# Kernel tuning notes

Hardware: AMD Instinct MI355X
Metric: run time of the kernel (lower is better)

The kernel has to match this reference:

```python
import jax, jax.numpy as jnp
import numpy as np

B, S, D, H = 2, 2048, 1024, 16
HD = D // H  # head dim = 64


def setup_inputs() -> dict:
    key = jax.random.key(0)
    ks = jax.random.split(key, 5)
    scale = 1.0 / np.sqrt(D)
    return {
        "hidden_states": jax.random.normal(ks[0], (B, S, D), jnp.float32),
        "attention_mask": jax.random.normal(ks[1], (B, 1, 1, S), jnp.float32),
        "Wq": jax.random.normal(ks[2], (D, D), jnp.float32) * scale,
        "bq": jnp.zeros((D,), jnp.float32),
        "Wk": jax.random.normal(ks[3], (D, D), jnp.float32) * scale,
        "bk": jnp.zeros((D,), jnp.float32),
        "Wv": jax.random.normal(ks[4], (D, D), jnp.float32) * scale,
        "bv": jnp.zeros((D,), jnp.float32),
    }


def _split_heads(x):
    # [B,S,D] -> [B,H,S,HD]
    return x.reshape(B, S, H, HD).transpose(0, 2, 1, 3)


def reference(hidden_states, attention_mask, Wq, bq, Wk, bk, Wv, bv):
    # torch Linear: y = x @ W.T + b
    q = _split_heads(hidden_states @ Wq.T + bq)
    k = _split_heads(hidden_states @ Wk.T + bk)
    v = _split_heads(hidden_states @ Wv.T + bv)

    scores = jnp.einsum("bhqd,bhkd->bhqk", q, k)
    # Faithful to source: with a mask present, the 1/sqrt(head_dim) scaling
    # is overwritten and raw scores are multiplied by the binary key mask.
    mask = (attention_mask >= 0).astype(scores.dtype)  # [B,1,1,S]
    probs = scores * mask
    # dropout prob = 0 (eval) -> identity

    ctx = jnp.einsum("bhqk,bhkd->bhqd", probs, v)
    ctx = ctx.transpose(0, 2, 1, 3).reshape(B, S, D)
    return ctx
```

## Files before the change

kernel.cpp:

```cpp
#include <hip/hip_runtime.h>

#define BB 2
#define SS 2048
#define DD 1024
#define HH 16
#define HDIM 64
#define MTOT 4096

typedef unsigned short u16;
typedef __bf16 bf16_t;
typedef bf16_t bf16x8 __attribute__((ext_vector_type(8)));
typedef float floatx4 __attribute__((ext_vector_type(4)));
typedef float floatx16 __attribute__((ext_vector_type(16)));

__device__ __forceinline__ float bf2f(u16 u) {
  union { unsigned int i; float f; } x;
  x.i = ((unsigned int)u) << 16;
  return x.f;
}
__device__ __forceinline__ u16 f2bf(float f) {
  union { float f; unsigned int i; } x;
  x.f = f;
  unsigned int r = x.i + 0x7fffu + ((x.i >> 16) & 1u);
  return (u16)(r >> 16);
}

__device__ __forceinline__ void gload16(const u16* g, u16* l) {
  __builtin_amdgcn_global_load_lds(
      (const __attribute__((address_space(1))) unsigned int*)g,
      (__attribute__((address_space(3))) unsigned int*)l, 16, 0, 0);
}

__global__ __launch_bounds__(256) void cast_to_bf16(
    const float* __restrict__ hs, const float* __restrict__ wq,
    const float* __restrict__ wk, const float* __restrict__ wv,
    u16* __restrict__ hs_b, u16* __restrict__ wq_b,
    u16* __restrict__ wk_b, u16* __restrict__ wv_b) {
  int fid = blockIdx.x * 256 + threadIdx.x;
  const float* src;
  u16* dst;
  int local;
  if (fid < 1048576) { src = hs; dst = hs_b; local = fid; }
  else if (fid < 1310720) { src = wq; dst = wq_b; local = fid - 1048576; }
  else if (fid < 1572864) { src = wk; dst = wk_b; local = fid - 1310720; }
  else { src = wv; dst = wv_b; local = fid - 1572864; }
  float4 v = reinterpret_cast<const float4*>(src)[local];
  ushort4 o;
  o.x = f2bf(v.x); o.y = f2bf(v.y); o.z = f2bf(v.z); o.w = f2bf(v.w);
  reinterpret_cast<ushort4*>(dst)[local] = o;
}

#define BKK 32
__global__ __launch_bounds__(256) void qkv_gemm_kernel(
    const u16* __restrict__ A,
    const u16* __restrict__ Wq, const u16* __restrict__ Wk, const u16* __restrict__ Wv,
    const float* __restrict__ bq, const float* __restrict__ bk, const float* __restrict__ bv,
    u16* __restrict__ Qo, u16* __restrict__ Ko, u16* __restrict__ Vo) {
  __shared__ u16 sA[128 * BKK];
  __shared__ u16 sB[128 * BKK];
  const int mt = blockIdx.y, ntall = blockIdx.x;
  const int seg = ntall >> 3, nt = ntall & 7;
  const u16* Wp = (seg == 0) ? Wq : (seg == 1) ? Wk : Wv;
  const float* bp = (seg == 0) ? bq : (seg == 1) ? bk : bv;
  u16* Out = (seg == 0) ? Qo : (seg == 1) ? Ko : Vo;
  const int m0 = mt * 128, n0 = nt * 128;
  const int tid = threadIdx.x;
  const int lane = tid & 63, wave = tid >> 6;
  const int wm = (wave >> 1) * 64, wn = (wave & 1) * 64;
  const int l32 = lane & 31, khalf = lane >> 5;
  const int grow = wave * 32 + l32;
  const int gcol = khalf * 8;
  floatx16 acc[2][2] = {};
  for (int k0 = 0; k0 < DD; k0 += BKK) {
#pragma unroll
    for (int c = 0; c < 2; ++c) {
      gload16(A + (size_t)(m0 + grow) * DD + k0 + c * 16 + gcol,
              sA + (wave * 128 + c * 64 + lane) * 8);
      gload16(Wp + (size_t)(n0 + grow) * DD + k0 + c * 16 + gcol,
              sB + (wave * 128 + c * 64 + lane) * 8);
    }
    __syncthreads();
#pragma unroll
    for (int kk = 0; kk < 2; ++kk) {
      bf16x8 af[2], bfr[2];
#pragma unroll
      for (int i = 0; i < 2; ++i) {
        int gA = (wave >> 1) * 2 + i;
        af[i] = *reinterpret_cast<const bf16x8*>(sA + (gA * 128 + kk * 64 + lane) * 8);
      }
#pragma unroll
      for (int j = 0; j < 2; ++j) {
        int gB = (wave & 1) * 2 + j;
        bfr[j] = *reinterpret_cast<const bf16x8*>(sB + (gB * 128 + kk * 64 + lane) * 8);
      }
#pragma unroll
      for (int i = 0; i < 2; ++i)
#pragma unroll
        for (int j = 0; j < 2; ++j)
          acc[i][j] = __builtin_amdgcn_mfma_f32_32x32x16_bf16(af[i], bfr[j], acc[i][j], 0, 0, 0);
    }
    __syncthreads();
  }
#pragma unroll
  for (int j = 0; j < 2; ++j) {
    int col = n0 + wn + j * 32 + l32;
    float bias = bp[col];
#pragma unroll
    for (int i = 0; i < 2; ++i) {
#pragma unroll
      for (int reg = 0; reg < 16; ++reg) {
        int row = m0 + wm + i * 32 + (reg & 3) + 8 * (reg >> 2) + 4 * khalf;
        Out[(size_t)row * DD + col] = f2bf(acc[i][j][reg] + bias);
      }
    }
  }
}

__global__ __launch_bounds__(256) void m_partial_kernel(
    const u16* __restrict__ Kb, const u16* __restrict__ Vb,
    const float* __restrict__ am, float* __restrict__ mpart) {
  __shared__ float sK[64 * 68];
  __shared__ float sV[64 * 68];
  const int bh = blockIdx.y;
  const int b = bh >> 4, h = bh & 15;
  const int tid = threadIdx.x;
  const int e0 = (tid & 15) * 4, d0 = (tid >> 4) * 4;
  float acc[4][4] = {};
  for (int cs = 0; cs < 4; ++cs) {
    const int s0 = (blockIdx.x * 4 + cs) * 64;
    if (cs) __syncthreads();
#pragma unroll
    for (int c = 0; c < 2; ++c) {
      int L = tid + c * 256;
      int srow = L >> 3;
      int col = (L & 7) * 8;
      size_t g = (size_t)(b * SS + s0 + srow) * DD + h * HDIM + col;
      uint4 kraw = *reinterpret_cast<const uint4*>(Kb + g);
      uint4 vraw = *reinterpret_cast<const uint4*>(Vb + g);
      float m = (am[b * SS + s0 + srow] >= 0.f) ? 1.f : 0.f;
      unsigned int kw[4] = {kraw.x, kraw.y, kraw.z, kraw.w};
      unsigned int vw[4] = {vraw.x, vraw.y, vraw.z, vraw.w};
#pragma unroll
      for (int q = 0; q < 4; ++q) {
        sK[srow * 68 + col + 2 * q]     = m * bf2f((u16)(kw[q] & 0xffffu));
        sK[srow * 68 + col + 2 * q + 1] = m * bf2f((u16)(kw[q] >> 16));
        sV[srow * 68 + col + 2 * q]     = bf2f((u16)(vw[q] & 0xffffu));
        sV[srow * 68 + col + 2 * q + 1] = bf2f((u16)(vw[q] >> 16));
      }
    }
    __syncthreads();
    for (int s = 0; s < 64; ++s) {
      float4 kk = *reinterpret_cast<const float4*>(&sK[s * 68 + e0]);
      float4 vv = *reinterpret_cast<const float4*>(&sV[s * 68 + d0]);
      float ka[4] = {kk.x, kk.y, kk.z, kk.w};
      float va[4] = {vv.x, vv.y, vv.z, vv.w};
#pragma unroll
      for (int i = 0; i < 4; ++i)
#pragma unroll
        for (int j = 0; j < 4; ++j) acc[i][j] += ka[i] * va[j];
    }
  }
  float* outp = mpart + ((size_t)(blockIdx.x * 32 + bh)) * 4096;
#pragma unroll
  for (int i = 0; i < 4; ++i) {
    float4 o = {acc[i][0], acc[i][1], acc[i][2], acc[i][3]};
    *reinterpret_cast<float4*>(&outp[(e0 + i) * 64 + d0]) = o;
  }
}

__global__ __launch_bounds__(256) void ctx_kernel(
    const u16* __restrict__ Qb, const float* __restrict__ mpart, float* __restrict__ Out) {
  __shared__ float sM[64 * 68];
  __shared__ float sQ[64 * 68];
  const int mchunk = blockIdx.x;
  const int h = blockIdx.y;
  const int m0 = mchunk * 64;
  const int b = m0 >> 11;
  const int bh = b * HH + h;
  const int tid = threadIdx.x;
#pragma unroll
  for (int c = 0; c < 4; ++c) {
    int L4 = c * 256 + tid;
    float4 s = {0.f, 0.f, 0.f, 0.f};
#pragma unroll
    for (int pc = 0; pc < 8; ++pc) {
      const float4* p4 = reinterpret_cast<const float4*>(mpart + ((size_t)(pc * 32 + bh)) * 4096);
      float4 t = p4[L4];
      s.x += t.x; s.y += t.y; s.z += t.z; s.w += t.w;
    }
    int e = L4 >> 4, d = (L4 & 15) * 4;
    *reinterpret_cast<float4*>(&sM[e * 68 + d]) = s;
  }
#pragma unroll
  for (int c = 0; c < 2; ++c) {
    int L = tid + c * 256;
    int row = L >> 3, col = (L & 7) * 8;
    uint4 q = *reinterpret_cast<const uint4*>(Qb + (size_t)(m0 + row) * DD + h * HDIM + col);
    unsigned int w[4] = {q.x, q.y, q.z, q.w};
#pragma unroll
    for (int t = 0; t < 4; ++t) {
      sQ[row * 68 + col + 2 * t]     = bf2f((u16)(w[t] & 0xffffu));
      sQ[row * 68 + col + 2 * t + 1] = bf2f((u16)(w[t] >> 16));
    }
  }
  __syncthreads();
  const int d0 = (tid & 15) * 4, ml0 = (tid >> 4) * 4;
  float acc[4][4] = {};
  for (int e4 = 0; e4 < 64; e4 += 4) {
    float4 mm[4], qq[4];
#pragma unroll
    for (int t = 0; t < 4; ++t)
      mm[t] = *reinterpret_cast<const float4*>(&sM[(e4 + t) * 68 + d0]);
#pragma unroll
    for (int i = 0; i < 4; ++i)
      qq[i] = *reinterpret_cast<const float4*>(&sQ[(ml0 + i) * 68 + e4]);
    float ma[4][4], qa[4][4];
#pragma unroll
    for (int t = 0; t < 4; ++t) {
      ma[t][0] = mm[t].x; ma[t][1] = mm[t].y; ma[t][2] = mm[t].z; ma[t][3] = mm[t].w;
      qa[t][0] = qq[t].x; qa[t][1] = qq[t].y; qa[t][2] = qq[t].z; qa[t][3] = qq[t].w;
    }
#pragma unroll
    for (int i = 0; i < 4; ++i)
#pragma unroll
      for (int t = 0; t < 4; ++t)
#pragma unroll
        for (int j = 0; j < 4; ++j)
          acc[i][j] += qa[i][t] * ma[t][j];
  }
#pragma unroll
  for (int i = 0; i < 4; ++i) {
    float4 o = {acc[i][0], acc[i][1], acc[i][2], acc[i][3]};
    *reinterpret_cast<float4*>(Out + (size_t)(m0 + ml0 + i) * DD + h * HDIM + d0) = o;
  }
}

extern "C" void kernel_launch(void* const* d_in, const int* in_sizes, int n_in,
                              void* d_out, int out_size, void* d_ws, size_t ws_size,
                              hipStream_t stream) {
  const float* hs = (const float*)d_in[0];
  const float* am = (const float*)d_in[1];
  const float* wq = (const float*)d_in[2];
  const float* bq = (const float*)d_in[3];
  const float* wk = (const float*)d_in[4];
  const float* bk = (const float*)d_in[5];
  const float* wv = (const float*)d_in[6];
  const float* bv = (const float*)d_in[7];
  float* out = (float*)d_out;
  char* ws = (char*)d_ws;

  u16* hs_b = (u16*)(ws);
  u16* wq_b = (u16*)(ws + 8388608);
  u16* wk_b = (u16*)(ws + 10485760);
  u16* wv_b = (u16*)(ws + 12582912);
  u16* q_b  = (u16*)(ws + 14680064);
  u16* k_b  = (u16*)(ws + 23068672);
  u16* v_b  = (u16*)(ws + 31457280);
  float* mpart = (float*)(ws + 39845888);

  cast_to_bf16<<<7168, 256, 0, stream>>>(hs, wq, wk, wv, hs_b, wq_b, wk_b, wv_b);
  qkv_gemm_kernel<<<dim3(24, 32), 256, 0, stream>>>(hs_b, wq_b, wk_b, wv_b,
                                                    bq, bk, bv, q_b, k_b, v_b);
  m_partial_kernel<<<dim3(8, 32), 256, 0, stream>>>(k_b, v_b, am, mpart);
  ctx_kernel<<<dim3(64, 16), 256, 0, stream>>>(q_b, mpart, out);
}
```

Measured before the change: 173.9 us.

## Cast inputs into k-panel layout for contiguous GEMM tile loads

The cast kernel now transposes the bf16 copies of hidden states and weights through shared memory into a panel layout ([K/8][rows][8]). The QKV GEMM loads each 16-byte k-chunk for consecutive rows from contiguous addresses instead of striding by the full row length. This is meant to coalesce the global-to-LDS loads, at the cost of a more complex cast kernel with an LDS transpose and a sync.

```diff
diff --git a/kernel.cpp b/kernel.cpp
--- a/kernel.cpp
+++ b/kernel.cpp
@@ -31,36 +31,53 @@
       (__attribute__((address_space(3))) unsigned int*)l, 16, 0, 0);
 }
 
-__global__ __launch_bounds__(256) void cast_to_bf16(
+__global__ __launch_bounds__(256) void cast_panel(
     const float* __restrict__ hs, const float* __restrict__ wq,
     const float* __restrict__ wk, const float* __restrict__ wv,
-    u16* __restrict__ hs_b, u16* __restrict__ wq_b,
-    u16* __restrict__ wk_b, u16* __restrict__ wv_b) {
-  int fid = blockIdx.x * 256 + threadIdx.x;
-  const float* src;
-  u16* dst;
-  int local;
-  if (fid < 1048576) { src = hs; dst = hs_b; local = fid; }
-  else if (fid < 1310720) { src = wq; dst = wq_b; local = fid - 1048576; }
-  else if (fid < 1572864) { src = wk; dst = wk_b; local = fid - 1310720; }
-  else { src = wv; dst = wv_b; local = fid - 1572864; }
-  float4 v = reinterpret_cast<const float4*>(src)[local];
-  ushort4 o;
-  o.x = f2bf(v.x); o.y = f2bf(v.y); o.z = f2bf(v.z); o.w = f2bf(v.w);
-  reinterpret_cast<ushort4*>(dst)[local] = o;
+    u16* __restrict__ hs_p, u16* __restrict__ wq_p,
+    u16* __restrict__ wk_p, u16* __restrict__ wv_p) {
+  __shared__ u16 sT[64 * 72];
+  const int bx = blockIdx.x, y = blockIdx.y;
+  const float* src; u16* dst; int r0, R;
+  if (bx < 64) { src = hs; dst = hs_p; r0 = bx * 64; R = 4096; }
+  else {
+    int w = (bx - 64) >> 4, t = (bx - 64) & 15;
+    src = (w == 0) ? wq : (w == 1) ? wk : wv;
+    dst = (w == 0) ? wq_p : (w == 1) ? wk_p : wv_p;
+    r0 = t * 64; R = 1024;
+  }
+  const int c0 = y * 64;
+  const int tid = threadIdx.x;
+#pragma unroll
+  for (int i = 0; i < 4; ++i) {
+    int e = i * 256 + tid;
+    int row = e >> 4, c4 = e & 15;
+    float4 v = reinterpret_cast<const float4*>(src)[(size_t)(r0 + row) * 256 + (c0 >> 2) + c4];
+    ushort4 o;
+    o.x = f2bf(v.x); o.y = f2bf(v.y); o.z = f2bf(v.z); o.w = f2bf(v.w);
+    *reinterpret_cast<ushort4*>(&sT[row * 72 + c4 * 4]) = o;
+  }
+  __syncthreads();
+#pragma unroll
+  for (int i = 0; i < 2; ++i) {
+    int e = i * 256 + tid;
+    int p = e >> 6, m = e & 63;
+    uint4 v = *reinterpret_cast<const uint4*>(&sT[m * 72 + p * 8]);
+    reinterpret_cast<uint4*>(dst)[(size_t)(y * 8 + p) * R + r0 + m] = v;
+  }
 }
 
 #define BKK 32
 __global__ __launch_bounds__(256) void qkv_gemm_kernel(
-    const u16* __restrict__ A,
-    const u16* __restrict__ Wq, const u16* __restrict__ Wk, const u16* __restrict__ Wv,
+    const u16* __restrict__ Ap,
+    const u16* __restrict__ Wqp, const u16* __restrict__ Wkp, const u16* __restrict__ Wvp,
     const float* __restrict__ bq, const float* __restrict__ bk, const float* __restrict__ bv,
     u16* __restrict__ Qo, u16* __restrict__ Ko, u16* __restrict__ Vo) {
   __shared__ u16 sA[128 * BKK];
   __shared__ u16 sB[128 * BKK];
   const int mt = blockIdx.y, ntall = blockIdx.x;
   const int seg = ntall >> 3, nt = ntall & 7;
-  const u16* Wp = (seg == 0) ? Wq : (seg == 1) ? Wk : Wv;
+  const u16* Wp = (seg == 0) ? Wqp : (seg == 1) ? Wkp : Wvp;
   const float* bp = (seg == 0) ? bq : (seg == 1) ? bk : bv;
   u16* Out = (seg == 0) ? Qo : (seg == 1) ? Ko : Vo;
   const int m0 = mt * 128, n0 = nt * 128;
@@ -68,16 +85,16 @@
   const int lane = tid & 63, wave = tid >> 6;
   const int wm = (wave >> 1) * 64, wn = (wave & 1) * 64;
   const int l32 = lane & 31, khalf = lane >> 5;
-  const int grow = wave * 32 + l32;
-  const int gcol = khalf * 8;
   floatx16 acc[2][2] = {};
   for (int k0 = 0; k0 < DD; k0 += BKK) {
+    const int p0 = k0 >> 3;
 #pragma unroll
     for (int c = 0; c < 2; ++c) {
-      gload16(A + (size_t)(m0 + grow) * DD + k0 + c * 16 + gcol,
-              sA + (wave * 128 + c * 64 + lane) * 8);
-      gload16(Wp + (size_t)(n0 + grow) * DD + k0 + c * 16 + gcol,
-              sB + (wave * 128 + c * 64 + lane) * 8);
+      const int pa = p0 + c * 2 + khalf;
+      gload16(Ap + ((size_t)pa * MTOT + m0 + wave * 32 + l32) * 8,
+              sA + ((wave * 2 + c) * 64 + lane) * 8);
+      gload16(Wp + ((size_t)pa * 1024 + n0 + wave * 32 + l32) * 8,
+              sB + ((wave * 2 + c) * 64 + lane) * 8);
     }
     __syncthreads();
 #pragma unroll
@@ -249,17 +266,17 @@
   float* out = (float*)d_out;
   char* ws = (char*)d_ws;
 
-  u16* hs_b = (u16*)(ws);
-  u16* wq_b = (u16*)(ws + 8388608);
-  u16* wk_b = (u16*)(ws + 10485760);
-  u16* wv_b = (u16*)(ws + 12582912);
+  u16* hs_p = (u16*)(ws);
+  u16* wq_p = (u16*)(ws + 8388608);
+  u16* wk_p = (u16*)(ws + 10485760);
+  u16* wv_p = (u16*)(ws + 12582912);
   u16* q_b  = (u16*)(ws + 14680064);
   u16* k_b  = (u16*)(ws + 23068672);
   u16* v_b  = (u16*)(ws + 31457280);
   float* mpart = (float*)(ws + 39845888);
 
-  cast_to_bf16<<<7168, 256, 0, stream>>>(hs, wq, wk, wv, hs_b, wq_b, wk_b, wv_b);
-  qkv_gemm_kernel<<<dim3(24, 32), 256, 0, stream>>>(hs_b, wq_b, wk_b, wv_b,
+  cast_panel<<<dim3(112, 16), 256, 0, stream>>>(hs, wq, wk, wv, hs_p, wq_p, wk_p, wv_p);
+  qkv_gemm_kernel<<<dim3(24, 32), 256, 0, stream>>>(hs_p, wq_p, wk_p, wv_p,
                                                     bq, bk, bv, q_b, k_b, v_b);
   m_partial_kernel<<<dim3(8, 32), 256, 0, stream>>>(k_b, v_b, am, mpart);
   ctx_kernel<<<dim3(64, 16), 256, 0, stream>>>(q_b, mpart, out);
```

Result: faster. 161.7 us (-7.0%).
